# Kernel optimization log

Measured on AMD Instinct MI355X. Metric: run time of the kernel, lower is better.

Reference implementation:

```python
import jax, jax.numpy as jnp
import numpy as np

B, N, D = 16384, 4, 256
EPS = 1e-5

# BatchNorm1d (training mode: batch stats, biased variance), applied on flattened (-1, feat)
def _bn(x, g, b):
    flat = x.reshape(-1, x.shape[-1])
    mu = jnp.mean(flat, axis=0)
    var = jnp.var(flat, axis=0)
    y = (flat - mu) * jax.lax.rsqrt(var + EPS) * g + b
    return y.reshape(x.shape)

# BaseMLP with one hidden layer: [BN -> Linear -> ReLU] -> [BN -> Linear -> Sigmoid]
def _mlp(x, g0, b0, W0, c0, g1, b1, W1, c1):
    h = jax.nn.relu(_bn(x, g0, b0) @ W0 + c0)
    return jax.nn.sigmoid(_bn(h, g1, b1) @ W1 + c1)


def setup_inputs() -> dict:
    key = jax.random.key(0)
    ks = iter(jax.random.split(key, 40))
    r = lambda shape, s: jax.random.normal(next(ks), shape, jnp.float32) * s
    inp = {"x": r((B, N, D), 1.0)}
    for p, (d0, d1, d2) in (("n", (D, 512, 256)), ("m", (2 * D, 512, 256)), ("f", (512, 512, 256))):
        inp[p + "g0"] = 1.0 + r((d0,), 0.1)
        inp[p + "b0"] = r((d0,), 0.1)
        inp[p + "W0"] = r((d0, d1), 0.05)
        inp[p + "c0"] = r((d1,), 0.01)
        inp[p + "g1"] = 1.0 + r((d1,), 0.1)
        inp[p + "b1"] = r((d1,), 0.1)
        inp[p + "W1"] = r((d1, d2), 0.05)
        inp[p + "c1"] = r((d2,), 0.01)
    return inp


def reference(x, ng0, nb0, nW0, nc0, ng1, nb1, nW1, nc1,
              mg0, mb0, mW0, mc0, mg1, mb1, mW1, mc1,
              fg0, fb0, fW0, fc0, fg1, fb1, fW1, fc1):
    # node transform: [B,4,D] -> [B,4,256]
    x_node = _mlp(x, ng0, nb0, nW0, nc0, ng1, nb1, nW1, nc1)
    # all ordered pairs (i,j), i!=j, in the original loop order
    pairs = [(i, j) for i in range(4) for j in range(4) if i != j]
    src = jnp.array([p[0] for p in pairs])  # [12]
    dst = jnp.array([p[1] for p in pairs])  # [12]
    msgs = jnp.concatenate([x[:, src, :], x[:, dst, :]], axis=-1)  # [B,12,2D]
    msgs = msgs.reshape(x.shape[0], 4, 3, 2 * x.shape[-1])
    x_msg = _mlp(msgs, mg0, mb0, mW0, mc0, mg1, mb1, mW1, mc1)  # [B,4,3,256]
    x_agg = jnp.mean(x_msg, axis=2)  # [B,4,256]
    out = _mlp(jnp.concatenate([x_node, x_agg], axis=-1), fg0, fb0, fW0, fc0, fg1, fb1, fW1, fc1)
    return out  # [B,4,256]
```

## Files before the change

kernel.cpp:

```cpp
#include <hip/hip_runtime.h>


typedef __attribute__((ext_vector_type(8))) short short8;
typedef __attribute__((ext_vector_type(4))) float f32x4;

__device__ __forceinline__ unsigned short f2bu(float f) {
    unsigned int x = __float_as_uint(f);
    x += 0x7fffu + ((x >> 16) & 1u);
    return (unsigned short)(x >> 16);
}
__device__ __forceinline__ float b2f(unsigned short u) {
    return __uint_as_float(((unsigned int)u) << 16);
}
__device__ __forceinline__ float sigmoidf_(float v) {
    return 1.0f / (1.0f + __expf(-v));
}

__global__ __launch_bounds__(256) void k_zero4(float4* p, int n4) {
    int i = blockIdx.x * 256 + threadIdx.x;
    if (i < n4) p[i] = make_float4(0.f, 0.f, 0.f, 0.f);
}

__global__ __launch_bounds__(256) void k_colstats(const float* __restrict__ x,
                                                  float* __restrict__ ssum,
                                                  float* __restrict__ ssq) {
    const int c = threadIdx.x;
    const int r0 = blockIdx.x * 64;
    float s = 0.f, q = 0.f;
    for (int r = r0; r < r0 + 64; ++r) {
        float v = x[(size_t)r * 256 + c];
        s += v; q += v * v;
    }
    atomicAdd(&ssum[c], s);
    atomicAdd(&ssq[c], q);
}

__global__ __launch_bounds__(256) void k_fold(const float* __restrict__ W,
                                              const float* __restrict__ gamma,
                                              const float* __restrict__ beta,
                                              const float* __restrict__ ssum,
                                              const float* __restrict__ ssq,
                                              const float* __restrict__ cvec,
                                              float inv_count, int N, int Kc,
                                              unsigned short* __restrict__ Bt,
                                              float* __restrict__ bias, int bias_add) {
    const int j = blockIdx.x;
    const int t = threadIdx.x;
    float part = 0.f;
    for (int k = t; k < Kc; k += 256) {
        float mu  = ssum[k] * inv_count;
        float var = ssq[k] * inv_count - mu * mu;
        float s   = gamma[k] * rsqrtf(var + 1e-5f);
        float tt  = beta[k] - mu * s;
        float w   = W[(size_t)k * N + j];
        Bt[(size_t)j * Kc + k] = f2bu(s * w);
        part += tt * w;
    }
    __shared__ float red[256];
    red[t] = part;
    __syncthreads();
    for (int s2 = 128; s2 > 0; s2 >>= 1) {
        if (t < s2) red[t] += red[t + s2];
        __syncthreads();
    }
    if (t == 0) {
        if (bias_add) atomicAdd(&bias[j], red[0]);
        else bias[j] = red[0] + cvec[j];
    }
}

__global__ __launch_bounds__(512) void k_msgstats(const unsigned short* __restrict__ PQ,
                                                  float* __restrict__ ssum,
                                                  float* __restrict__ ssq) {
    const int f = threadIdx.x;
    float s = 0.f, q = 0.f;
    const int r0 = blockIdx.x * 48;
    for (int r = r0; r < r0 + 48; ++r) {
        int b  = r / 12;
        int p  = r - b * 12;
        int si = p / 3;
        int t  = p - si * 3;
        int di = t + (t >= si ? 1 : 0);
        float pv = b2f(PQ[(size_t)(b * 4 + si) * 1024 + f]);
        float qv = b2f(PQ[(size_t)(b * 4 + di) * 1024 + 512 + f]);
        float v = fmaxf(pv + qv, 0.f);
        s += v; q += v * v;
    }
    atomicAdd(&ssum[f], s);
    atomicAdd(&ssq[f], q);
}

__global__ __launch_bounds__(256) void k_aggfin(const float* __restrict__ agg,
                                                unsigned short* __restrict__ inf_,
                                                float* __restrict__ ssum,
                                                float* __restrict__ ssq) {
    const int f = threadIdx.x;
    const int g0 = blockIdx.x * 64;
    float s = 0.f, q = 0.f;
    for (int g = g0; g < g0 + 64; ++g) {
        float v = agg[(size_t)g * 256 + f];
        inf_[(size_t)g * 512 + 256 + f] = f2bu(v);
        s += v; q += v * v;
    }
    atomicAdd(&ssum[f], s);
    atomicAdd(&ssq[f], q);
}

template <int EPI, int AF32>
__global__ __launch_bounds__(256) void k_gemm(const void* __restrict__ Av, int lda,
                                              const unsigned short* __restrict__ Bt,
                                              void* __restrict__ C, int ldc,
                                              const float* __restrict__ bias,
                                              float* __restrict__ ssum, float* __restrict__ ssq,
                                              int K) {
    const int n0 = blockIdx.x * 128;
    const int m0 = blockIdx.y * 128;
    const int tid = threadIdx.x;
    const int w = tid >> 6;
    const int lane = tid & 63;
    const int q = lane >> 4;
    const int l = lane & 15;
    const int wm = w >> 1;
    const int wn = w & 1;

    __shared__ __align__(16) unsigned short lA[128 * 32];
    __shared__ __align__(16) unsigned short lB[128 * 32];
    __shared__ float s_sum[128];
    __shared__ float s_sq[128];

    if ((EPI == 1 || EPI == 2) && tid < 128) { s_sum[tid] = 0.f; s_sq[tid] = 0.f; }

    f32x4 acc[4][4] = {};

    const int rsub = tid >> 2;
    const int ksub = (tid & 3) * 8;
    const unsigned short* gA16 = (const unsigned short*)Av + (size_t)(m0 + rsub) * lda + ksub;
    const float*          gA32 = (const float*)Av + (size_t)(m0 + rsub) * lda + ksub;
    const unsigned short* gB = Bt + (size_t)(n0 + rsub) * K + ksub;
    unsigned short* wA = lA + rsub * 32 + ksub;
    unsigned short* wB = lB + rsub * 32 + ksub;

    for (int k0 = 0; k0 < K; k0 += 32) {
        short8 a8[2], b8[2];
#pragma unroll
        for (int t = 0; t < 2; ++t) {
            if (AF32) {
                float4 f0 = *(const float4*)(gA32 + (size_t)t * 64 * lda + k0);
                float4 f1 = *(const float4*)(gA32 + (size_t)t * 64 * lda + k0 + 4);
                short8 o;
                o[0] = (short)f2bu(f0.x); o[1] = (short)f2bu(f0.y);
                o[2] = (short)f2bu(f0.z); o[3] = (short)f2bu(f0.w);
                o[4] = (short)f2bu(f1.x); o[5] = (short)f2bu(f1.y);
                o[6] = (short)f2bu(f1.z); o[7] = (short)f2bu(f1.w);
                a8[t] = o;
            } else {
                a8[t] = *(const short8*)(gA16 + (size_t)t * 64 * lda + k0);
            }
            b8[t] = *(const short8*)(gB + (size_t)t * 64 * K + k0);
        }
        __syncthreads();
#pragma unroll
        for (int t = 0; t < 2; ++t) {
            *(short8*)(wA + t * 64 * 32) = a8[t];
            *(short8*)(wB + t * 64 * 32) = b8[t];
        }
        __syncthreads();
        short8 av[4], bv[4];
#pragma unroll
        for (int i = 0; i < 4; ++i)
            av[i] = *(const short8*)(lA + ((wm * 64 + i * 16 + l) * 32 + q * 8));
#pragma unroll
        for (int j = 0; j < 4; ++j)
            bv[j] = *(const short8*)(lB + ((wn * 64 + j * 16 + l) * 32 + q * 8));
#pragma unroll
        for (int i = 0; i < 4; ++i)
#pragma unroll
            for (int j = 0; j < 4; ++j)
                acc[i][j] = __builtin_amdgcn_mfma_f32_16x16x32_bf16(av[i], bv[j], acc[i][j], 0, 0, 0);
    }

#pragma unroll
    for (int j = 0; j < 4; ++j) {
        const int colL = wn * 64 + j * 16 + l;
        const int col = n0 + colL;
        const float bb = bias[col];
        float psum = 0.f, psq = 0.f;
#pragma unroll
        for (int i = 0; i < 4; ++i) {
            const int rowL = wm * 64 + i * 16 + q * 4;
#pragma unroll
            for (int r = 0; r < 4; ++r) {
                float v = acc[i][j][r] + bb;
                if (EPI == 1) v = fmaxf(v, 0.f);
                if (EPI == 2 || EPI == 4) v = sigmoidf_(v);
                const size_t off = (size_t)(m0 + rowL + r) * ldc + col;
                if (EPI == 4) ((float*)C)[off] = v;
                else ((unsigned short*)C)[off] = f2bu(v);
                psum += v; psq += v * v;
            }
        }
        if (EPI == 1 || EPI == 2) {
            atomicAdd(&s_sum[colL], psum);
            atomicAdd(&s_sq[colL], psq);
        }
    }
    if (EPI == 1 || EPI == 2) {
        __syncthreads();
        if (tid < 128) {
            atomicAdd(&ssum[n0 + tid], s_sum[tid]);
            atomicAdd(&ssq[n0 + tid], s_sq[tid]);
        }
    }
}

__global__ __launch_bounds__(256) void k_gemm_msg(const unsigned short* __restrict__ PQ,
                                                  const unsigned short* __restrict__ Bt,
                                                  float* __restrict__ agg,
                                                  const float* __restrict__ bias) {
    const int K = 512;
    const int n0 = blockIdx.x * 128;
    const int m0 = blockIdx.y * 128;
    const int tid = threadIdx.x;
    const int w = tid >> 6;
    const int lane = tid & 63;
    const int q = lane >> 4;
    const int l = lane & 15;
    const int wm = w >> 1;
    const int wn = w & 1;

    __shared__ __align__(16) unsigned short lA[128 * 32];
    __shared__ __align__(16) unsigned short lB[128 * 32];

    f32x4 acc[4][4] = {};

    const int rsub = tid >> 2;
    const int ksub = (tid & 3) * 8;
    size_t aP[2], aQ[2];
#pragma unroll
    for (int t = 0; t < 2; ++t) {
        int r = m0 + t * 64 + rsub;
        int b = r / 12;
        int p = r - b * 12;
        int si = p / 3;
        int tt = p - si * 3;
        int di = tt + (tt >= si ? 1 : 0);
        aP[t] = (size_t)(b * 4 + si) * 1024 + ksub;
        aQ[t] = (size_t)(b * 4 + di) * 1024 + 512 + ksub;
    }
    const unsigned short* gB = Bt + (size_t)(n0 + rsub) * K + ksub;
    unsigned short* wA = lA + rsub * 32 + ksub;
    unsigned short* wB = lB + rsub * 32 + ksub;

    for (int k0 = 0; k0 < K; k0 += 32) {
        short8 a8[2], b8[2];
#pragma unroll
        for (int t = 0; t < 2; ++t) {
            short8 p8 = *(const short8*)(PQ + aP[t] + k0);
            short8 q8 = *(const short8*)(PQ + aQ[t] + k0);
            short8 o;
#pragma unroll
            for (int e = 0; e < 8; ++e) {
                float v = b2f((unsigned short)p8[e]) + b2f((unsigned short)q8[e]);
                o[e] = (short)f2bu(fmaxf(v, 0.f));
            }
            a8[t] = o;
            b8[t] = *(const short8*)(gB + (size_t)t * 64 * K + k0);
        }
        __syncthreads();
#pragma unroll
        for (int t = 0; t < 2; ++t) {
            *(short8*)(wA + t * 64 * 32) = a8[t];
            *(short8*)(wB + t * 64 * 32) = b8[t];
        }
        __syncthreads();
        short8 av[4], bv[4];
#pragma unroll
        for (int i = 0; i < 4; ++i)
            av[i] = *(const short8*)(lA + ((wm * 64 + i * 16 + l) * 32 + q * 8));
#pragma unroll
        for (int j = 0; j < 4; ++j)
            bv[j] = *(const short8*)(lB + ((wn * 64 + j * 16 + l) * 32 + q * 8));
#pragma unroll
        for (int i = 0; i < 4; ++i)
#pragma unroll
            for (int j = 0; j < 4; ++j)
                acc[i][j] = __builtin_amdgcn_mfma_f32_16x16x32_bf16(av[i], bv[j], acc[i][j], 0, 0, 0);
    }

#pragma unroll
    for (int j = 0; j < 4; ++j) {
        const int col = n0 + wn * 64 + j * 16 + l;
        const float bb = bias[col];
#pragma unroll
        for (int i = 0; i < 4; ++i) {
            const int rowL = wm * 64 + i * 16 + q * 4;
#pragma unroll
            for (int r = 0; r < 4; ++r) {
                float v = sigmoidf_(acc[i][j][r] + bb);
                const int row = m0 + rowL + r;
                atomicAdd(&agg[(size_t)(row / 3) * 256 + col], v * (1.f / 3.f));
            }
        }
    }
}

extern "C" void kernel_launch(void* const* d_in, const int* in_sizes, int n_in,
                              void* d_out, int out_size, void* d_ws, size_t ws_size,
                              hipStream_t stream) {
    const float* x   = (const float*)d_in[0];
    const float* ng0 = (const float*)d_in[1];
    const float* nb0 = (const float*)d_in[2];
    const float* nW0 = (const float*)d_in[3];
    const float* nc0 = (const float*)d_in[4];
    const float* ng1 = (const float*)d_in[5];
    const float* nb1 = (const float*)d_in[6];
    const float* nW1 = (const float*)d_in[7];
    const float* nc1 = (const float*)d_in[8];
    const float* mg0 = (const float*)d_in[9];
    const float* mb0 = (const float*)d_in[10];
    const float* mW0 = (const float*)d_in[11];
    const float* mc0 = (const float*)d_in[12];
    const float* mg1 = (const float*)d_in[13];
    const float* mb1 = (const float*)d_in[14];
    const float* mW1 = (const float*)d_in[15];
    const float* mc1 = (const float*)d_in[16];
    const float* fg0 = (const float*)d_in[17];
    const float* fb0 = (const float*)d_in[18];
    const float* fW0 = (const float*)d_in[19];
    const float* fc0 = (const float*)d_in[20];
    const float* fg1 = (const float*)d_in[21];
    const float* fb1 = (const float*)d_in[22];
    const float* fW1 = (const float*)d_in[23];
    const float* fc1 = (const float*)d_in[24];

    char* ws = (char*)d_ws;
    const size_t MiB = 1024 * 1024;

    int Cq = 1;
    while (Cq < 8 && (68 + 128 / Cq) * MiB > ws_size) Cq *= 2;
    const int G = 65536 / Cq;

    float* stat = (float*)ws;
    float* sx_s   = stat + 0;
    float* sx_q   = stat + 256;
    float* shn_s  = stat + 512;
    float* shn_q  = stat + 1024;
    float* shm_s  = stat + 1536;
    float* shm_q  = stat + 2048;
    float* sif_s  = stat + 2560;
    float* sif_q  = stat + 3072;
    float* shf_s  = stat + 3584;
    float* shf_q  = stat + 4096;
    float* biasPQ = stat + 4608;
    float* bias_n = stat + 5632;
    float* b1n    = stat + 6144;
    float* b1m    = stat + 6400;
    float* b0f    = stat + 6656;
    float* b1f    = stat + 7168;

    unsigned short* An  = (unsigned short*)(ws + 256 * 1024);
    unsigned short* Btm = An + 512 * 256;
    unsigned short* A1n = Btm + 1024 * 256;
    unsigned short* A1m = A1n + 256 * 512;
    unsigned short* A0f = A1m + 256 * 512;
    unsigned short* A1f = A0f + 512 * 512;

    unsigned short* hn    = (unsigned short*)(ws + 4 * MiB);
    float*          agg   = (float*)(ws + 4 * MiB);
    unsigned short* hf    = (unsigned short*)(ws + 4 * MiB);
    unsigned short* PQbuf = (unsigned short*)(ws + 68 * MiB);
    unsigned short* inf   = (unsigned short*)d_out;

    const float inv1 = 1.f / 65536.f;
    const float invM = 1.f / 196608.f;

    k_zero4<<<6, 256, 0, stream>>>((float4*)stat, 1408);

    k_colstats<<<1024, 256, 0, stream>>>(x, sx_s, sx_q);

    k_fold<<<512, 256, 0, stream>>>(nW0, ng0, nb0, sx_s, sx_q, nc0, inv1, 512, 256, An, bias_n, 0);
    k_fold<<<512, 256, 0, stream>>>(mW0, mg0, mb0, sx_s, sx_q, mc0, inv1, 512, 256, Btm, biasPQ, 0);
    k_fold<<<512, 256, 0, stream>>>(mW0 + 256 * 512, mg0 + 256, mb0 + 256, sx_s, sx_q, nullptr,
                                    inv1, 512, 256, Btm + 512 * 256, biasPQ, 1);

    k_gemm<1, 1><<<dim3(4, 512), 256, 0, stream>>>(x, 256, An, hn, 512, bias_n, shn_s, shn_q, 256);

    for (int c = 0; c < Cq; ++c) {
        k_gemm<5, 1><<<dim3(8, 512 / Cq), 256, 0, stream>>>(
            x + (size_t)c * G * 256, 256, Btm, PQbuf, 1024, biasPQ, nullptr, nullptr, 256);
        k_msgstats<<<4096 / Cq, 512, 0, stream>>>(PQbuf, shm_s, shm_q);
    }

    k_fold<<<256, 256, 0, stream>>>(nW1, ng1, nb1, shn_s, shn_q, nc1, inv1, 256, 512, A1n, b1n, 0);
    k_fold<<<256, 256, 0, stream>>>(mW1, mg1, mb1, shm_s, shm_q, mc1, invM, 256, 512, A1m, b1m, 0);

    k_gemm<2, 0><<<dim3(2, 512), 256, 0, stream>>>(hn, 512, A1n, inf, 512, b1n, sif_s, sif_q, 512);

    k_zero4<<<16384, 256, 0, stream>>>((float4*)agg, 4194304);
    for (int c = 0; c < Cq; ++c) {
        if (Cq > 1)
            k_gemm<5, 1><<<dim3(8, 512 / Cq), 256, 0, stream>>>(
                x + (size_t)c * G * 256, 256, Btm, PQbuf, 1024, biasPQ, nullptr, nullptr, 256);
        k_gemm_msg<<<dim3(2, 1536 / Cq), 256, 0, stream>>>(PQbuf, A1m, agg + (size_t)c * G * 256, b1m);
    }
    k_aggfin<<<1024, 256, 0, stream>>>(agg, inf, sif_s + 256, sif_q + 256);

    k_fold<<<512, 256, 0, stream>>>(fW0, fg0, fb0, sif_s, sif_q, fc0, inv1, 512, 512, A0f, b0f, 0);
    k_gemm<1, 0><<<dim3(4, 512), 256, 0, stream>>>(inf, 512, A0f, hf, 512, b0f, shf_s, shf_q, 512);
    k_fold<<<256, 256, 0, stream>>>(fW1, fg1, fb1, shf_s, shf_q, fc1, inv1, 256, 512, A1f, b1f, 0);
    k_gemm<4, 0><<<dim3(2, 512), 256, 0, stream>>>(hf, 512, A1f, d_out, 256, b1f, nullptr, nullptr, 512);

    (void)in_sizes; (void)n_in; (void)out_size;
}
```

Baseline: 917.6 us.

## Use direct global-to-LDS loads and widen message GEMM tile to full N

```diff
diff --git a/kernel.cpp b/kernel.cpp
--- a/kernel.cpp
+++ b/kernel.cpp
@@ -1,8 +1,10 @@
 #include <hip/hip_runtime.h>
+#include <hip/hip_bf16.h>
 
 
 typedef __attribute__((ext_vector_type(8))) short short8;
 typedef __attribute__((ext_vector_type(4))) float f32x4;
+typedef __attribute__((ext_vector_type(4))) unsigned int uint4v;
 
 __device__ __forceinline__ unsigned short f2bu(float f) {
     unsigned int x = __float_as_uint(f);
@@ -14,6 +16,19 @@
 }
 __device__ __forceinline__ float sigmoidf_(float v) {
     return 1.0f / (1.0f + __expf(-v));
+}
+__device__ __forceinline__ unsigned int pk2(float a, float b) {
+    __hip_bfloat162 h = __float22bfloat162_rn(make_float2(a, b));
+    unsigned int u;
+    __builtin_memcpy(&u, &h, 4);
+    return u;
+}
+
+__device__ __forceinline__ void load_lds16(const void* g, void* l) {
+    __builtin_amdgcn_global_load_lds(
+        (__attribute__((address_space(1))) unsigned int*)(uintptr_t)g,
+        (__attribute__((address_space(3))) unsigned int*)(uintptr_t)l,
+        16, 0, 0);
 }
 
 __global__ __launch_bounds__(256) void k_zero4(float4* p, int n4) {
@@ -137,32 +152,32 @@
     const unsigned short* gA16 = (const unsigned short*)Av + (size_t)(m0 + rsub) * lda + ksub;
     const float*          gA32 = (const float*)Av + (size_t)(m0 + rsub) * lda + ksub;
     const unsigned short* gB = Bt + (size_t)(n0 + rsub) * K + ksub;
+    unsigned short* lA_wave = lA + w * 512;
+    unsigned short* lB_wave = lB + w * 512;
     unsigned short* wA = lA + rsub * 32 + ksub;
-    unsigned short* wB = lB + rsub * 32 + ksub;
 
     for (int k0 = 0; k0 < K; k0 += 32) {
-        short8 a8[2], b8[2];
-#pragma unroll
-        for (int t = 0; t < 2; ++t) {
-            if (AF32) {
+        uint4v a4[2];
+        if (AF32) {
+#pragma unroll
+            for (int t = 0; t < 2; ++t) {
                 float4 f0 = *(const float4*)(gA32 + (size_t)t * 64 * lda + k0);
                 float4 f1 = *(const float4*)(gA32 + (size_t)t * 64 * lda + k0 + 4);
-                short8 o;
-                o[0] = (short)f2bu(f0.x); o[1] = (short)f2bu(f0.y);
-                o[2] = (short)f2bu(f0.z); o[3] = (short)f2bu(f0.w);
-                o[4] = (short)f2bu(f1.x); o[5] = (short)f2bu(f1.y);
-                o[6] = (short)f2bu(f1.z); o[7] = (short)f2bu(f1.w);
-                a8[t] = o;
-            } else {
-                a8[t] = *(const short8*)(gA16 + (size_t)t * 64 * lda + k0);
+                a4[t] = uint4v{pk2(f0.x, f0.y), pk2(f0.z, f0.w),
+                               pk2(f1.x, f1.y), pk2(f1.z, f1.w)};
             }
-            b8[t] = *(const short8*)(gB + (size_t)t * 64 * K + k0);
-        }
-        __syncthreads();
-#pragma unroll
-        for (int t = 0; t < 2; ++t) {
-            *(short8*)(wA + t * 64 * 32) = a8[t];
-            *(short8*)(wB + t * 64 * 32) = b8[t];
+        } else {
+#pragma unroll
+            for (int t = 0; t < 2; ++t)
+                load_lds16(gA16 + (size_t)t * 64 * lda + k0, lA_wave + t * 2048);
+        }
+#pragma unroll
+        for (int t = 0; t < 2; ++t)
+            load_lds16(gB + (size_t)t * 64 * K + k0, lB_wave + t * 2048);
+        if (AF32) {
+#pragma unroll
+            for (int t = 0; t < 2; ++t)
+                *(uint4v*)(wA + t * 64 * 32) = a4[t];
         }
         __syncthreads();
         short8 av[4], bv[4];
@@ -177,6 +192,7 @@
 #pragma unroll
             for (int j = 0; j < 4; ++j)
                 acc[i][j] = __builtin_amdgcn_mfma_f32_16x16x32_bf16(av[i], bv[j], acc[i][j], 0, 0, 0);
+        __syncthreads();
     }
 
 #pragma unroll
@@ -218,8 +234,7 @@
                                                   float* __restrict__ agg,
                                                   const float* __restrict__ bias) {
     const int K = 512;
-    const int n0 = blockIdx.x * 128;
-    const int m0 = blockIdx.y * 128;
+    const int m0 = blockIdx.x * 128;
     const int tid = threadIdx.x;
     const int w = tid >> 6;
     const int lane = tid & 63;
@@ -229,9 +244,9 @@
     const int wn = w & 1;
 
     __shared__ __align__(16) unsigned short lA[128 * 32];
-    __shared__ __align__(16) unsigned short lB[128 * 32];
-
-    f32x4 acc[4][4] = {};
+    __shared__ __align__(16) unsigned short lB[256 * 32];
+
+    f32x4 acc[4][8] = {};
 
     const int rsub = tid >> 2;
     const int ksub = (tid & 3) * 8;
@@ -247,59 +262,62 @@
         aP[t] = (size_t)(b * 4 + si) * 1024 + ksub;
         aQ[t] = (size_t)(b * 4 + di) * 1024 + 512 + ksub;
     }
-    const unsigned short* gB = Bt + (size_t)(n0 + rsub) * K + ksub;
+    const unsigned short* gB = Bt + (size_t)rsub * K + ksub;
+    unsigned short* lB_wave = lB + w * 512;
     unsigned short* wA = lA + rsub * 32 + ksub;
-    unsigned short* wB = lB + rsub * 32 + ksub;
 
     for (int k0 = 0; k0 < K; k0 += 32) {
-        short8 a8[2], b8[2];
+        uint4v a4[2];
 #pragma unroll
         for (int t = 0; t < 2; ++t) {
             short8 p8 = *(const short8*)(PQ + aP[t] + k0);
             short8 q8 = *(const short8*)(PQ + aQ[t] + k0);
-            short8 o;
-#pragma unroll
-            for (int e = 0; e < 8; ++e) {
-                float v = b2f((unsigned short)p8[e]) + b2f((unsigned short)q8[e]);
-                o[e] = (short)f2bu(fmaxf(v, 0.f));
-            }
-            a8[t] = o;
-            b8[t] = *(const short8*)(gB + (size_t)t * 64 * K + k0);
-        }
-        __syncthreads();
-#pragma unroll
-        for (int t = 0; t < 2; ++t) {
-            *(short8*)(wA + t * 64 * 32) = a8[t];
-            *(short8*)(wB + t * 64 * 32) = b8[t];
-        }
-        __syncthreads();
-        short8 av[4], bv[4];
+            float v[8];
+#pragma unroll
+            for (int e = 0; e < 8; ++e)
+                v[e] = fmaxf(b2f((unsigned short)p8[e]) + b2f((unsigned short)q8[e]), 0.f);
+            a4[t] = uint4v{pk2(v[0], v[1]), pk2(v[2], v[3]),
+                           pk2(v[4], v[5]), pk2(v[6], v[7])};
+        }
+#pragma unroll
+        for (int t = 0; t < 4; ++t)
+            load_lds16(gB + (size_t)t * 64 * K + k0, lB_wave + t * 2048);
+#pragma unroll
+        for (int t = 0; t < 2; ++t)
+            *(uint4v*)(wA + t * 64 * 32) = a4[t];
+        __syncthreads();
+        short8 av[4], bv[8];
 #pragma unroll
         for (int i = 0; i < 4; ++i)
             av[i] = *(const short8*)(lA + ((wm * 64 + i * 16 + l) * 32 + q * 8));
 #pragma unroll
-        for (int j = 0; j < 4; ++j)
-            bv[j] = *(const short8*)(lB + ((wn * 64 + j * 16 + l) * 32 + q * 8));
+        for (int j = 0; j < 8; ++j)
+            bv[j] = *(const short8*)(lB + ((wn * 128 + j * 16 + l) * 32 + q * 8));
 #pragma unroll
         for (int i = 0; i < 4; ++i)
 #pragma unroll
-            for (int j = 0; j < 4; ++j)
+            for (int j = 0; j < 8; ++j)
                 acc[i][j] = __builtin_amdgcn_mfma_f32_16x16x32_bf16(av[i], bv[j], acc[i][j], 0, 0, 0);
-    }
-
-#pragma unroll
-    for (int j = 0; j < 4; ++j) {
-        const int col = n0 + wn * 64 + j * 16 + l;
-        const float bb = bias[col];
-#pragma unroll
-        for (int i = 0; i < 4; ++i) {
-            const int rowL = wm * 64 + i * 16 + q * 4;
+        __syncthreads();
+    }
+
+#pragma unroll
+    for (int i = 0; i < 4; ++i) {
+        const int base = m0 + wm * 64 + i * 16 + q * 4;
+        const int node0 = base / 3;
+        const int nfirst = 3 - (base - node0 * 3);
+#pragma unroll
+        for (int j = 0; j < 8; ++j) {
+            const int col = wn * 128 + j * 16 + l;
+            const float bb = bias[col];
+            float v0 = 0.f, v1 = 0.f;
 #pragma unroll
             for (int r = 0; r < 4; ++r) {
                 float v = sigmoidf_(acc[i][j][r] + bb);
-                const int row = m0 + rowL + r;
-                atomicAdd(&agg[(size_t)(row / 3) * 256 + col], v * (1.f / 3.f));
+                if (r < nfirst) v0 += v; else v1 += v;
             }
+            atomicAdd(&agg[(size_t)node0 * 256 + col], v0 * (1.f / 3.f));
+            atomicAdd(&agg[(size_t)(node0 + 1) * 256 + col], v1 * (1.f / 3.f));
         }
     }
 }
@@ -375,7 +393,6 @@
     const float invM = 1.f / 196608.f;
 
     k_zero4<<<6, 256, 0, stream>>>((float4*)stat, 1408);
-
     k_colstats<<<1024, 256, 0, stream>>>(x, sx_s, sx_q);
 
     k_fold<<<512, 256, 0, stream>>>(nW0, ng0, nb0, sx_s, sx_q, nc0, inv1, 512, 256, An, bias_n, 0);
@@ -401,7 +418,7 @@
         if (Cq > 1)
             k_gemm<5, 1><<<dim3(8, 512 / Cq), 256, 0, stream>>>(
                 x + (size_t)c * G * 256, 256, Btm, PQbuf, 1024, biasPQ, nullptr, nullptr, 256);
-        k_gemm_msg<<<dim3(2, 1536 / Cq), 256, 0, stream>>>(PQbuf, A1m, agg + (size_t)c * G * 256, b1m);
+        k_gemm_msg<<<1536 / Cq, 256, 0, stream>>>(PQbuf, A1m, agg + (size_t)c * G * 256, b1m);
     }
     k_aggfin<<<1024, 256, 0, stream>>>(agg, inf, sif_s + 256, sif_q + 256);
 
```

Result: slower. 948.3 us (+3.3%).
